# Optimization experiments

Hardware: AMD Instinct MI355X
Metric: run time of the kernel (lower is better)

## Reference

```python
import jax, jax.numpy as jnp
import numpy as np

B, N, D = 4, 2048, 1024
H = 16
d_head = D // H
N_CTX = 512


def setup_inputs() -> dict:
    key = jax.random.key(0)
    ks = jax.random.split(key, 6)
    x = jax.random.normal(ks[0], (B, N, D), dtype=jnp.float32)
    ctx_ppr = jax.random.uniform(ks[1], (N_CTX,), dtype=jnp.float32)
    ctx_trust = jax.random.normal(ks[2], (N_CTX,), dtype=jnp.float32)
    W_in = jax.random.normal(ks[3], (3 * D, D), dtype=jnp.float32) * (D ** -0.5)
    b_in = jnp.zeros((3 * D,), dtype=jnp.float32)
    W_out = jax.random.normal(ks[4], (D, D), dtype=jnp.float32) * (D ** -0.5)
    b_out = jnp.zeros((D,), dtype=jnp.float32)
    log_ppr_alpha = jnp.ones((1,), dtype=jnp.float32) * 0.1
    trust_scale = jnp.ones((1,), dtype=jnp.float32) * 0.1
    return {
        "x": x, "n_ctx": N_CTX, "ctx_ppr": ctx_ppr, "ctx_trust": ctx_trust,
        "W_in": W_in, "b_in": b_in, "W_out": W_out, "b_out": b_out,
        "log_ppr_alpha": log_ppr_alpha, "trust_scale": trust_scale,
    }


def reference(x, n_ctx, ctx_ppr, ctx_trust, W_in, b_in, W_out, b_out,
              log_ppr_alpha, trust_scale):
    Bn, Nn, Dn = x.shape
    scale = d_head ** -0.5
    # fused QKV projection: [B,N,3D]
    qkv = jnp.einsum('bnd,ed->bne', x, W_in) + b_in
    q, k, v = jnp.split(qkv, 3, axis=-1)
    # [B,H,N,d]
    def to_heads(t):
        return t.reshape(Bn, Nn, H, d_head).transpose(0, 2, 1, 3)
    q, k, v = to_heads(q), to_heads(k), to_heads(v)
    if n_ctx > 0:
        # sigmoid value gate on the first n_ctx (context) key positions
        gate = jax.nn.sigmoid(trust_scale * ctx_trust)  # [n_ctx]
        gate_full = jnp.concatenate([gate, jnp.ones((Nn - n_ctx,), x.dtype)])
        v = v * gate_full[None, None, :, None]
    logits = jnp.einsum('bhqd,bhkd->bhqk', q, k) * scale
    if n_ctx > 0:
        # additive per-key log-PPR bias on context columns
        col_bias = -log_ppr_alpha * jnp.log(jnp.clip(ctx_ppr, 1e-8))  # [n_ctx]
        col_bias_full = jnp.concatenate([col_bias, jnp.zeros((Nn - n_ctx,), x.dtype)])
        logits = logits + col_bias_full[None, None, None, :]
    weights = jax.nn.softmax(logits, axis=-1)  # dropout: eval mode (identity)
    out = jnp.einsum('bhqk,bhkd->bhqd', weights, v)
    out = out.transpose(0, 2, 1, 3).reshape(Bn, Nn, Dn)
    return jnp.einsum('bnd,ed->bne', out, W_out) + b_out
```

## Files before the change

kernel.cpp:

```cpp
#include <hip/hip_runtime.h>
#include <math.h>

typedef unsigned short u16;
typedef unsigned int   u32;
typedef __attribute__((ext_vector_type(8))) short short8;
typedef __attribute__((ext_vector_type(4))) float floatx4;

#define MFMA16(a, b, c) __builtin_amdgcn_mfma_f32_16x16x32_bf16(a, b, c, 0, 0, 0)
#define LOG2E 1.4426950408889634f

__device__ __forceinline__ float b2f(u16 b) { return __uint_as_float(((u32)b) << 16); }
__device__ __forceinline__ u16 f2b(float f) {
  u32 x = __float_as_uint(f);
  return (u16)((x + 0x7FFFu + ((x >> 16) & 1u)) >> 16);
}
__device__ __forceinline__ float fexp2(float x) {
  float r;
  asm("v_exp_f32 %0, %1" : "=v"(r) : "v"(x));
  return r;
}
__device__ __forceinline__ short8 pack8(float4 a, float4 b) {
  short8 r;
  r[0] = (short)f2b(a.x); r[1] = (short)f2b(a.y); r[2] = (short)f2b(a.z); r[3] = (short)f2b(a.w);
  r[4] = (short)f2b(b.x); r[5] = (short)f2b(b.y); r[6] = (short)f2b(b.z); r[7] = (short)f2b(b.w);
  return r;
}
__device__ __forceinline__ void gload16(const u16* g, u16* l) {
  __builtin_amdgcn_global_load_lds(
      (const __attribute__((address_space(1))) u32*)g,
      (__attribute__((address_space(3))) u32*)l, 16, 0, 0);
}

__global__ void prep_kernel(const float* __restrict__ ppr, const float* __restrict__ trust,
                            const float* __restrict__ plpa, const float* __restrict__ ptsc,
                            const int* __restrict__ pnc,
                            float* __restrict__ colbias, float* __restrict__ vgate)
{
  const int i = blockIdx.x * 256 + threadIdx.x;
  const int n_ctx = pnc[0];
  const float lpa = plpa[0], ts = ptsc[0];
  if (i < 2048) {
    float cb = 0.0f, g = 1.0f;
    if (i < n_ctx) {
      cb = -lpa * logf(fmaxf(ppr[i], 1e-8f)) * LOG2E;
      g = 1.0f / (1.0f + expf(-ts * trust[i]));
    }
    colbias[i] = cb;
    vgate[i] = g;
  }
}

__global__ __launch_bounds__(256) void convert1(const float* __restrict__ X, const float* __restrict__ Wi,
                                                u16* __restrict__ Xb, u16* __restrict__ Wib)
{
  const size_t i = ((size_t)blockIdx.x * 256 + threadIdx.x) * 8;
  const float* src;
  u16* dst;
  if (i < 8388608) { src = X + i; dst = Xb + i; }
  else { src = Wi + (i - 8388608); dst = Wib + (i - 8388608); }
  float4 a = *(const float4*)src, b = *(const float4*)(src + 4);
  *(short8*)dst = pack8(a, b);
}

__global__ __launch_bounds__(256) void convert2(const float* __restrict__ Wo, u16* __restrict__ Wob)
{
  const size_t i = ((size_t)blockIdx.x * 256 + threadIdx.x) * 8;
  float4 a = *(const float4*)(Wo + i), b = *(const float4*)(Wo + i + 4);
  *(short8*)(Wob + i) = pack8(a, b);
}

__global__ __launch_bounds__(256) void qkv_mfma(
    const u16* __restrict__ Xb, const u16* __restrict__ Wib, const float* __restrict__ bin,
    const float* __restrict__ vgate,
    u16* __restrict__ qW, u16* __restrict__ kW, u16* __restrict__ vT)
{
  __shared__ __align__(16) u16 SMEM[8704];
  u16* As = SMEM;
  u16* Bs = SMEM + 4096;
  const int tid = threadIdx.x;
  const int wave = tid >> 6, lane = tid & 63;
  const int k15 = lane & 15, quad = lane >> 4;
  const int wm = wave & 1, wn = wave >> 1;
  const int m0 = blockIdx.y << 7, n0 = blockIdx.x << 7;

  const int r0 = (wave << 5) + (lane >> 2);
  const int cc = (lane & 3) << 3;
  const u16* gA = Xb + (size_t)(m0 + r0) * 1024 + cc;
  const u16* gB = Wib + (size_t)(n0 + r0) * 1024 + cc;
  u16* lA = As + (wave << 10);
  u16* lB = Bs + (wave << 10);

  floatx4 c[4][4];
#pragma unroll
  for (int i = 0; i < 4; ++i)
#pragma unroll
    for (int j = 0; j < 4; ++j) c[i][j] = (floatx4){0.f, 0.f, 0.f, 0.f};

  for (int k0 = 0; k0 < 1024; k0 += 32) {
    __syncthreads();
    gload16(gA + k0, lA);
    gload16(gA + k0 + 16 * 1024, lA + 512);
    gload16(gB + k0, lB);
    gload16(gB + k0 + 16 * 1024, lB + 512);
    __syncthreads();
    short8 af[4], bf[4];
#pragma unroll
    for (int rt = 0; rt < 4; ++rt)
      af[rt] = *(const short8*)(As + (64 * wm + 16 * rt + k15) * 32 + quad * 8);
#pragma unroll
    for (int ct = 0; ct < 4; ++ct)
      bf[ct] = *(const short8*)(Bs + (64 * wn + 16 * ct + k15) * 32 + quad * 8);
#pragma unroll
    for (int rt = 0; rt < 4; ++rt)
#pragma unroll
      for (int ct = 0; ct < 4; ++ct)
        c[rt][ct] = MFMA16(af[rt], bf[ct], c[rt][ct]);
  }

  const int which = n0 >> 10;
  if (which < 2) {
    u16* dst0 = which ? kW : qW;
    const float ksc = which ? 0.125f * LOG2E : 1.0f;
#pragma unroll
    for (int ct = 0; ct < 4; ++ct) {
      const int e = n0 + 64 * wn + 16 * ct + k15;
      const float bb = bin[e];
      const int h = (e >> 6) & 15, d = e & 63;
#pragma unroll
      for (int rt = 0; rt < 4; ++rt)
#pragma unroll
        for (int r = 0; r < 4; ++r) {
          const int m = m0 + 64 * wm + 16 * rt + 4 * quad + r;
          const int b = m >> 11, n = m & 2047;
          dst0[(((size_t)(b * 16 + h)) * 2048 + n) * 64 + d] = f2b((c[rt][ct][r] + bb) * ksc);
        }
    }
  } else {
    const int b = m0 >> 11, nbase = m0 & 2047;
    u16* T = SMEM;
    for (int half = 0; half < 2; ++half) {
      __syncthreads();
      if (wn == half) {
#pragma unroll
        for (int ct = 0; ct < 4; ++ct) {
          const int el = 16 * ct + k15;
          const int e = n0 + 64 * half + el;
          const float bb = bin[e];
#pragma unroll
          for (int rt = 0; rt < 4; ++rt)
#pragma unroll
            for (int r = 0; r < 4; ++r) {
              const int ml = 64 * wm + 16 * rt + 4 * quad + r;
              T[el * 136 + ml] = f2b((c[rt][ct][r] + bb) * vgate[nbase + ml]);
            }
        }
      }
      __syncthreads();
#pragma unroll
      for (int uu = 0; uu < 4; ++uu) {
        const int u = tid + uu * 256;
        const int el = u >> 4, moct = u & 15;
        const int e = n0 + 64 * half + el;
        const int h = (e >> 6) & 15, d = e & 63;
        short8 vv = *(const short8*)(T + el * 136 + moct * 8);
        *(short8*)(vT + (((size_t)(b * 16 + h)) * 64 + d) * 2048 + nbase + moct * 8) = vv;
      }
    }
  }
}

__global__ __launch_bounds__(256, 4) void attn_mfma(
    const u16* __restrict__ qW, const u16* __restrict__ kW, const u16* __restrict__ vT,
    const float* __restrict__ colbias, u16* __restrict__ aO)
{
  __shared__ __align__(16) u16 Kbuf[2][4096];
  __shared__ __align__(16) u16 Vbuf[2][4096];
  __shared__ __align__(16) u16 Ps[4][1024];

  const int tid = threadIdx.x;
  const int wave = tid >> 6, lane = tid & 63;
  const int k15 = lane & 15, quad = lane >> 4;
  const int bid = blockIdx.x;
  const int bh = bid & 63, qt = bid >> 6;
  const size_t base = (size_t)bh * 2048 * 64;
  const size_t baseV = (size_t)bh * 64 * 2048;
  const int q0 = qt * 128 + wave * 32;

  const int sw3 = (k15 & 7) << 3;
  const int cA = (quad * 8) ^ sw3;
  const int cB = (quad * 8 + 32) ^ sw3;

  const int krow0 = wave * 16 + (lane >> 3);
  const int swz = ((lane & 7) * 8) ^ ((lane >> 3) << 3);
  const u16* gK = kW + base + (size_t)krow0 * 64 + swz;
  const u16* gV = vT + baseV + (size_t)krow0 * 2048 + swz;

#define STAGE(nb, kbn) do {                                                    \
    gload16(gK + (size_t)(kbn) * 64, &Kbuf[nb][wave * 1024]);                  \
    gload16(gK + (size_t)(kbn) * 64 + 512, &Kbuf[nb][wave * 1024 + 512]);      \
    gload16(gV + (kbn), &Vbuf[nb][wave * 1024]);                               \
    gload16(gV + (kbn) + 8 * 2048, &Vbuf[nb][wave * 1024 + 512]);              \
  } while (0)

  const u16* qp = qW + base + (size_t)(q0 + k15) * 64 + quad * 8;
  short8 qa00 = *(const short8*)qp;
  short8 qa01 = *(const short8*)(qp + 32);
  short8 qa10 = *(const short8*)(qp + 16 * 64);
  short8 qa11 = *(const short8*)(qp + 16 * 64 + 32);

  floatx4 o0[4], o1[4];
#pragma unroll
  for (int t = 0; t < 4; ++t) {
    o0[t] = (floatx4){0.f, 0.f, 0.f, 0.f};
    o1[t] = (floatx4){0.f, 0.f, 0.f, 0.f};
  }
  floatx4 l0 = (floatx4){0.f, 0.f, 0.f, 0.f};
  floatx4 l1 = (floatx4){0.f, 0.f, 0.f, 0.f};
  float m0 = -3.0e38f, m1 = -3.0e38f;

  u16* PsW = Ps[wave];
  const short8 ones8 = (short8){16256, 16256, 16256, 16256, 16256, 16256, 16256, 16256};

  STAGE(0, 0);

  for (int kb = 0; kb < 2048; kb += 64) {
    const int cur = (kb >> 6) & 1;

    float4 cb[4];
#pragma unroll
    for (int t = 0; t < 4; ++t)
      cb[t] = *(const float4*)(colbias + kb + 16 * t + 4 * quad);
    __builtin_amdgcn_sched_barrier(0);
    if (kb < 1984) {
      STAGE(cur ^ 1, kb + 64);
      asm volatile("s_waitcnt vmcnt(4)" ::: "memory");
    } else {
      asm volatile("s_waitcnt vmcnt(0)" ::: "memory");
    }
    __builtin_amdgcn_sched_barrier(0);
    __builtin_amdgcn_s_barrier();
    __builtin_amdgcn_sched_barrier(0);

    const u16* Kc = Kbuf[cur];
    const u16* Vc = Vbuf[cur];

    floatx4 s0[4], s1[4];
    __builtin_amdgcn_s_setprio(1);
#pragma unroll
    for (int t = 0; t < 4; ++t) {
      const u16* kp = Kc + (16 * t + k15) * 64;
      short8 ka0 = *(const short8*)(kp + cA);
      short8 ka1 = *(const short8*)(kp + cB);
      floatx4 ci = (floatx4){cb[t].x, cb[t].y, cb[t].z, cb[t].w};
      s0[t] = MFMA16(ka0, qa00, ci);
      s0[t] = MFMA16(ka1, qa01, s0[t]);
      s1[t] = MFMA16(ka0, qa10, ci);
      s1[t] = MFMA16(ka1, qa11, s1[t]);
    }
    __builtin_amdgcn_s_setprio(0);

#define SOFTHALF(S, M, L, O) do {                                              \
    float mx = fmaxf(fmaxf(S[0][0], S[0][1]), fmaxf(S[0][2], S[0][3]));        \
    _Pragma("unroll") for (int t = 1; t < 4; ++t)                              \
      mx = fmaxf(mx, fmaxf(fmaxf(S[t][0], S[t][1]), fmaxf(S[t][2], S[t][3]))); \
    mx = fmaxf(mx, __shfl_xor(mx, 16));                                        \
    mx = fmaxf(mx, __shfl_xor(mx, 32));                                        \
    if (__any(mx > (M) + 8.0f)) {                                              \
      const float mn = fmaxf(M, mx);                                           \
      const float al = fexp2((M) - mn);                                        \
      M = mn;                                                                  \
      const float a0 = __shfl(al, 4 * quad + 0);                               \
      const float a1 = __shfl(al, 4 * quad + 1);                               \
      const float a2 = __shfl(al, 4 * quad + 2);                               \
      const float a3 = __shfl(al, 4 * quad + 3);                               \
      L[0] *= a0; L[1] *= a1; L[2] *= a2; L[3] *= a3;                          \
      _Pragma("unroll") for (int t = 0; t < 4; ++t) {                          \
        O[t][0] *= a0; O[t][1] *= a1; O[t][2] *= a2; O[t][3] *= a3;            \
      }                                                                        \
    }                                                                          \
    _Pragma("unroll") for (int t = 0; t < 4; ++t) {                            \
      float p0 = fexp2(S[t][0] - M), p1 = fexp2(S[t][1] - M);                  \
      float p2 = fexp2(S[t][2] - M), p3 = fexp2(S[t][3] - M);                  \
      u32 lo = __builtin_amdgcn_perm(__float_as_uint(p1), __float_as_uint(p0), 0x07060302u); \
      u32 hi = __builtin_amdgcn_perm(__float_as_uint(p3), __float_as_uint(p2), 0x07060302u); \
      *(uint2*)(PsW + k15 * 64 + ((16 * t + 4 * quad) ^ sw3)) = (uint2){lo, hi}; \
    }                                                                          \
  } while (0)

    SOFTHALF(s0, m0, l0, o0);
    short8 pa00 = *(const short8*)(PsW + k15 * 64 + cA);
    short8 pa01 = *(const short8*)(PsW + k15 * 64 + cB);
    {
      floatx4 z4 = (floatx4){0.f, 0.f, 0.f, 0.f};
      floatx4 sA = MFMA16(pa00, ones8, z4);
      sA = MFMA16(pa01, ones8, sA);
      l0 += sA;
    }
    SOFTHALF(s1, m1, l1, o1);
    short8 pa10 = *(const short8*)(PsW + k15 * 64 + cA);
    short8 pa11 = *(const short8*)(PsW + k15 * 64 + cB);
    {
      floatx4 z4 = (floatx4){0.f, 0.f, 0.f, 0.f};
      floatx4 sB = MFMA16(pa10, ones8, z4);
      sB = MFMA16(pa11, ones8, sB);
      l1 += sB;
    }

    __builtin_amdgcn_s_setprio(1);
#pragma unroll
    for (int t = 0; t < 4; ++t) {
      const u16* vp = Vc + (16 * t + k15) * 64;
      short8 vb0 = *(const short8*)(vp + cA);
      short8 vb1 = *(const short8*)(vp + cB);
      o0[t] = MFMA16(pa00, vb0, o0[t]);
      o0[t] = MFMA16(pa01, vb1, o0[t]);
      o1[t] = MFMA16(pa10, vb0, o1[t]);
      o1[t] = MFMA16(pa11, vb1, o1[t]);
    }
    __builtin_amdgcn_s_setprio(0);
    __builtin_amdgcn_sched_barrier(0);
    __builtin_amdgcn_s_barrier();
    __builtin_amdgcn_sched_barrier(0);
  }
#undef SOFTHALF
#undef STAGE

  const int b = bh >> 4, h = bh & 15;
#pragma unroll
  for (int r = 0; r < 4; ++r) {
    {
      const int q = q0 + 4 * quad + r;
      const float inv = 1.0f / l0[r];
      u16* dst = aO + (size_t)(b * 2048 + q) * 1024 + h * 64;
#pragma unroll
      for (int t = 0; t < 4; ++t) dst[16 * t + k15] = f2b(o0[t][r] * inv);
    }
    {
      const int q = q0 + 16 + 4 * quad + r;
      const float inv = 1.0f / l1[r];
      u16* dst = aO + (size_t)(b * 2048 + q) * 1024 + h * 64;
#pragma unroll
      for (int t = 0; t < 4; ++t) dst[16 * t + k15] = f2b(o1[t][r] * inv);
    }
  }
}

__global__ __launch_bounds__(256) void oproj_mfma(
    const u16* __restrict__ A, const u16* __restrict__ Wob, const float* __restrict__ bout,
    float* __restrict__ out)
{
  __shared__ __align__(16) u16 SMEM[8192];
  u16* As = SMEM;
  u16* Bs = SMEM + 4096;
  const int tid = threadIdx.x;
  const int wave = tid >> 6, lane = tid & 63;
  const int k15 = lane & 15, quad = lane >> 4;
  const int wm = wave & 1, wn = wave >> 1;
  const int m0 = blockIdx.y << 7, n0 = blockIdx.x << 7;

  const int r0 = (wave << 5) + (lane >> 2);
  const int cc = (lane & 3) << 3;
  const u16* gA = A + (size_t)(m0 + r0) * 1024 + cc;
  const u16* gB = Wob + (size_t)(n0 + r0) * 1024 + cc;
  u16* lA = As + (wave << 10);
  u16* lB = Bs + (wave << 10);

  floatx4 c[4][4];
#pragma unroll
  for (int i = 0; i < 4; ++i)
#pragma unroll
    for (int j = 0; j < 4; ++j) c[i][j] = (floatx4){0.f, 0.f, 0.f, 0.f};

  for (int k0 = 0; k0 < 1024; k0 += 32) {
    __syncthreads();
    gload16(gA + k0, lA);
    gload16(gA + k0 + 16 * 1024, lA + 512);
    gload16(gB + k0, lB);
    gload16(gB + k0 + 16 * 1024, lB + 512);
    __syncthreads();
    short8 af[4], bf[4];
#pragma unroll
    for (int rt = 0; rt < 4; ++rt)
      af[rt] = *(const short8*)(As + (64 * wm + 16 * rt + k15) * 32 + quad * 8);
#pragma unroll
    for (int ct = 0; ct < 4; ++ct)
      bf[ct] = *(const short8*)(Bs + (64 * wn + 16 * ct + k15) * 32 + quad * 8);
#pragma unroll
    for (int rt = 0; rt < 4; ++rt)
#pragma unroll
      for (int ct = 0; ct < 4; ++ct)
        c[rt][ct] = MFMA16(af[rt], bf[ct], c[rt][ct]);
  }

#pragma unroll
  for (int ct = 0; ct < 4; ++ct) {
    const int e = n0 + 64 * wn + 16 * ct + k15;
    const float bb = bout[e];
#pragma unroll
    for (int rt = 0; rt < 4; ++rt)
#pragma unroll
      for (int r = 0; r < 4; ++r) {
        const int m = m0 + 64 * wm + 16 * rt + 4 * quad + r;
        out[(size_t)m * 1024 + e] = c[rt][ct][r] + bb;
      }
  }
}

extern "C" void kernel_launch(void* const* d_in, const int* in_sizes, int n_in,
                              void* d_out, int out_size, void* d_ws, size_t ws_size,
                              hipStream_t stream)
{
  const float* X     = (const float*)d_in[0];
  const int*   pnc   = (const int*)d_in[1];
  const float* ppr   = (const float*)d_in[2];
  const float* trust = (const float*)d_in[3];
  const float* Win   = (const float*)d_in[4];
  const float* bin   = (const float*)d_in[5];
  const float* Wout  = (const float*)d_in[6];
  const float* bout  = (const float*)d_in[7];
  const float* plpa  = (const float*)d_in[8];
  const float* ptsc  = (const float*)d_in[9];
  float* out = (float*)d_out;

  const size_t SZ = (size_t)64 * 2048 * 64;
  u16* Xb = (u16*)d_ws;
  u16* qW = Xb + SZ;
  u16* kW = qW + SZ;
  u16* vT = kW + SZ;
  u16* aO = Xb;
  u16* Wob = kW;
  float* colbias = (float*)d_out;
  float* vgate   = colbias + 2048;
  u16*   Wib     = (u16*)(vgate + 2048);

  prep_kernel<<<dim3(8), 256, 0, stream>>>(ppr, trust, plpa, ptsc, pnc, colbias, vgate);
  convert1<<<dim3(5632), 256, 0, stream>>>(X, Win, Xb, Wib);
  qkv_mfma<<<dim3(24, 64), 256, 0, stream>>>(Xb, Wib, bin, vgate, qW, kW, vT);
  attn_mfma<<<dim3(1024), 256, 0, stream>>>(qW, kW, vT, colbias, aO);
  convert2<<<dim3(512), 256, 0, stream>>>(Wout, Wob);
  oproj_mfma<<<dim3(8, 64), 256, 0, stream>>>(aO, Wob, bout, out);
}
```

Measured before the change: 353.1 us.

## Double-buffer LDS with swizzled layout in QKV and output projection GEMMs

Both projection GEMMs now prefetch the next K-slice into a second LDS buffer with global_load_lds while MFMAs run on the current one. Manual vmcnt waits and raw barriers replace the two __syncthreads per iteration. An XOR swizzle is applied to the global-to-LDS mapping and to the fragment reads to avoid LDS bank conflicts, and wave priority is raised around the MFMA block. This hides global load latency at the cost of doubling LDS per block, which may reduce occupancy.

After: 316.7 us. -10.3%, faster.

```diff
diff --git a/kernel.cpp b/kernel.cpp
--- a/kernel.cpp
+++ b/kernel.cpp
@@ -29,6 +29,9 @@
   __builtin_amdgcn_global_load_lds(
       (const __attribute__((address_space(1))) u32*)g,
       (__attribute__((address_space(3))) u32*)l, 16, 0, 0);
+}
+__device__ __forceinline__ int swzg(int r, int c) {
+  return ((r >> 1) << 6) + (((((r & 1) << 2) | c) ^ ((r >> 1) & 7)) << 3);
 }
 
 __global__ void prep_kernel(const float* __restrict__ ppr, const float* __restrict__ trust,
@@ -74,21 +77,27 @@
     const float* __restrict__ vgate,
     u16* __restrict__ qW, u16* __restrict__ kW, u16* __restrict__ vT)
 {
-  __shared__ __align__(16) u16 SMEM[8704];
-  u16* As = SMEM;
-  u16* Bs = SMEM + 4096;
+  __shared__ __align__(16) u16 SMEM[16384];
   const int tid = threadIdx.x;
   const int wave = tid >> 6, lane = tid & 63;
   const int k15 = lane & 15, quad = lane >> 4;
   const int wm = wave & 1, wn = wave >> 1;
   const int m0 = blockIdx.y << 7, n0 = blockIdx.x << 7;
 
-  const int r0 = (wave << 5) + (lane >> 2);
-  const int cc = (lane & 3) << 3;
-  const u16* gA = Xb + (size_t)(m0 + r0) * 1024 + cc;
-  const u16* gB = Wib + (size_t)(n0 + r0) * 1024 + cc;
-  u16* lA = As + (wave << 10);
-  u16* lB = Bs + (wave << 10);
+  const int line = lane >> 3;
+  const int sl = (lane & 7) ^ line;
+  const int rloc = (line << 1) | (sl >> 2);
+  const int cch = (sl & 3) << 3;
+  const u16* gA = Xb + (size_t)(m0 + (wave << 5) + rloc) * 1024 + cch;
+  const u16* gB = Wib + (size_t)(n0 + (wave << 5) + rloc) * 1024 + cch;
+
+#define STAGE(buf, k0s) do {                                                   \
+    u16* As_ = SMEM + (buf) * 8192 + (wave << 10);                             \
+    gload16(gA + (k0s), As_);                                                  \
+    gload16(gA + (k0s) + 16 * 1024, As_ + 512);                                \
+    gload16(gB + (k0s), As_ + 4096);                                           \
+    gload16(gB + (k0s) + 16 * 1024, As_ + 4608);                               \
+  } while (0)
 
   floatx4 c[4][4];
 #pragma unroll
@@ -96,26 +105,42 @@
 #pragma unroll
     for (int j = 0; j < 4; ++j) c[i][j] = (floatx4){0.f, 0.f, 0.f, 0.f};
 
+  STAGE(0, 0);
   for (int k0 = 0; k0 < 1024; k0 += 32) {
-    __syncthreads();
-    gload16(gA + k0, lA);
-    gload16(gA + k0 + 16 * 1024, lA + 512);
-    gload16(gB + k0, lB);
-    gload16(gB + k0 + 16 * 1024, lB + 512);
-    __syncthreads();
+    const int cur = (k0 >> 5) & 1;
+    if (k0 < 992) {
+      STAGE(cur ^ 1, k0 + 32);
+      __builtin_amdgcn_sched_barrier(0);
+      asm volatile("s_waitcnt vmcnt(4)" ::: "memory");
+    } else {
+      __builtin_amdgcn_sched_barrier(0);
+      asm volatile("s_waitcnt vmcnt(0)" ::: "memory");
+    }
+    __builtin_amdgcn_sched_barrier(0);
+    __builtin_amdgcn_s_barrier();
+    __builtin_amdgcn_sched_barrier(0);
+
+    const u16* Asc = SMEM + cur * 8192;
+    const u16* Bsc = Asc + 4096;
     short8 af[4], bf[4];
 #pragma unroll
     for (int rt = 0; rt < 4; ++rt)
-      af[rt] = *(const short8*)(As + (64 * wm + 16 * rt + k15) * 32 + quad * 8);
+      af[rt] = *(const short8*)(Asc + swzg(64 * wm + 16 * rt + k15, quad));
 #pragma unroll
     for (int ct = 0; ct < 4; ++ct)
-      bf[ct] = *(const short8*)(Bs + (64 * wn + 16 * ct + k15) * 32 + quad * 8);
+      bf[ct] = *(const short8*)(Bsc + swzg(64 * wn + 16 * ct + k15, quad));
+    __builtin_amdgcn_s_setprio(1);
 #pragma unroll
     for (int rt = 0; rt < 4; ++rt)
 #pragma unroll
       for (int ct = 0; ct < 4; ++ct)
         c[rt][ct] = MFMA16(af[rt], bf[ct], c[rt][ct]);
-  }
+    __builtin_amdgcn_s_setprio(0);
+    __builtin_amdgcn_sched_barrier(0);
+    __builtin_amdgcn_s_barrier();
+    __builtin_amdgcn_sched_barrier(0);
+  }
+#undef STAGE
 
   const int which = n0 >> 10;
   if (which < 2) {
@@ -349,21 +374,27 @@
     const u16* __restrict__ A, const u16* __restrict__ Wob, const float* __restrict__ bout,
     float* __restrict__ out)
 {
-  __shared__ __align__(16) u16 SMEM[8192];
-  u16* As = SMEM;
-  u16* Bs = SMEM + 4096;
+  __shared__ __align__(16) u16 SMEM[16384];
   const int tid = threadIdx.x;
   const int wave = tid >> 6, lane = tid & 63;
   const int k15 = lane & 15, quad = lane >> 4;
   const int wm = wave & 1, wn = wave >> 1;
   const int m0 = blockIdx.y << 7, n0 = blockIdx.x << 7;
 
-  const int r0 = (wave << 5) + (lane >> 2);
-  const int cc = (lane & 3) << 3;
-  const u16* gA = A + (size_t)(m0 + r0) * 1024 + cc;
-  const u16* gB = Wob + (size_t)(n0 + r0) * 1024 + cc;
-  u16* lA = As + (wave << 10);
-  u16* lB = Bs + (wave << 10);
+  const int line = lane >> 3;
+  const int sl = (lane & 7) ^ line;
+  const int rloc = (line << 1) | (sl >> 2);
+  const int cch = (sl & 3) << 3;
+  const u16* gA = A + (size_t)(m0 + (wave << 5) + rloc) * 1024 + cch;
+  const u16* gB = Wob + (size_t)(n0 + (wave << 5) + rloc) * 1024 + cch;
+
+#define STAGE(buf, k0s) do {                                                   \
+    u16* As_ = SMEM + (buf) * 8192 + (wave << 10);                             \
+    gload16(gA + (k0s), As_);                                                  \
+    gload16(gA + (k0s) + 16 * 1024, As_ + 512);                                \
+    gload16(gB + (k0s), As_ + 4096);                                           \
+    gload16(gB + (k0s) + 16 * 1024, As_ + 4608);                               \
+  } while (0)
 
   floatx4 c[4][4];
 #pragma unroll
@@ -371,26 +402,42 @@
 #pragma unroll
     for (int j = 0; j < 4; ++j) c[i][j] = (floatx4){0.f, 0.f, 0.f, 0.f};
 
+  STAGE(0, 0);
   for (int k0 = 0; k0 < 1024; k0 += 32) {
-    __syncthreads();
-    gload16(gA + k0, lA);
-    gload16(gA + k0 + 16 * 1024, lA + 512);
-    gload16(gB + k0, lB);
-    gload16(gB + k0 + 16 * 1024, lB + 512);
-    __syncthreads();
+    const int cur = (k0 >> 5) & 1;
+    if (k0 < 992) {
+      STAGE(cur ^ 1, k0 + 32);
+      __builtin_amdgcn_sched_barrier(0);
+      asm volatile("s_waitcnt vmcnt(4)" ::: "memory");
+    } else {
+      __builtin_amdgcn_sched_barrier(0);
+      asm volatile("s_waitcnt vmcnt(0)" ::: "memory");
+    }
+    __builtin_amdgcn_sched_barrier(0);
+    __builtin_amdgcn_s_barrier();
+    __builtin_amdgcn_sched_barrier(0);
+
+    const u16* Asc = SMEM + cur * 8192;
+    const u16* Bsc = Asc + 4096;
     short8 af[4], bf[4];
 #pragma unroll
     for (int rt = 0; rt < 4; ++rt)
-      af[rt] = *(const short8*)(As + (64 * wm + 16 * rt + k15) * 32 + quad * 8);
+      af[rt] = *(const short8*)(Asc + swzg(64 * wm + 16 * rt + k15, quad));
 #pragma unroll
     for (int ct = 0; ct < 4; ++ct)
-      bf[ct] = *(const short8*)(Bs + (64 * wn + 16 * ct + k15) * 32 + quad * 8);
+      bf[ct] = *(const short8*)(Bsc + swzg(64 * wn + 16 * ct + k15, quad));
+    __builtin_amdgcn_s_setprio(1);
 #pragma unroll
     for (int rt = 0; rt < 4; ++rt)
 #pragma unroll
       for (int ct = 0; ct < 4; ++ct)
         c[rt][ct] = MFMA16(af[rt], bf[ct], c[rt][ct]);
-  }
+    __builtin_amdgcn_s_setprio(0);
+    __builtin_amdgcn_sched_barrier(0);
+    __builtin_amdgcn_s_barrier();
+    __builtin_amdgcn_sched_barrier(0);
+  }
+#undef STAGE
 
 #pragma unroll
   for (int ct = 0; ct < 4; ++ct) {
```
